# Kernel optimization log

Measured on AMD Instinct MI355X. Metric: run time of the kernel, lower is better.

## Reference

```python
import jax, jax.numpy as jnp
import numpy as np

N = 50000   # nodes
E = 800000  # edges
DIN, DH, DOUT = 128, 128, 128


def _w(k, o, i):
    return jax.random.normal(k, (o, i), jnp.float32) * (1.0 / np.sqrt(i))


def setup_inputs() -> dict:
    key = jax.random.key(0)
    ks = jax.random.split(key, 16)
    return {
        "x": jax.random.normal(ks[0], (N, DIN), jnp.float32),
        "edge_index": jax.random.randint(ks[1], (2, E), 0, N, dtype=jnp.int64),
        # conv1 = GraphSAGE(DIN, DH, num_layers=2): two SAGEConv layers
        "W1l": _w(ks[2], DH, DIN), "W1r": _w(ks[3], DH, DIN), "b1": jnp.zeros((DH,), jnp.float32),
        "W2l": _w(ks[4], DH, DH),  "W2r": _w(ks[5], DH, DH),  "b2": jnp.zeros((DH,), jnp.float32),
        # conv2 = GraphSAGE(DH, DOUT, num_layers=2)
        "W3l": _w(ks[6], DOUT, DH),   "W3r": _w(ks[7], DOUT, DH),   "b3": jnp.zeros((DOUT,), jnp.float32),
        "W4l": _w(ks[8], DOUT, DOUT), "W4r": _w(ks[9], DOUT, DOUT), "b4": jnp.zeros((DOUT,), jnp.float32),
        # final fc
        "Wfc": _w(ks[10], DOUT, DOUT), "bfc": jnp.zeros((DOUT,), jnp.float32),
    }


def _sage(x, src, dst, Wl, Wr, b):
    # PyG SAGEConv (aggr='mean'): out = lin_l(mean_{j in N(i)} x_j) + lin_r(x_i)
    agg = jax.ops.segment_sum(x[src], dst, num_segments=N)          # [N, F]
    cnt = jax.ops.segment_sum(jnp.ones((src.shape[0],), x.dtype), dst, num_segments=N)
    mean = agg / jnp.maximum(cnt, 1.0)[:, None]                     # isolated nodes -> 0
    return mean @ Wl.T + x @ Wr.T + b


def reference(x, edge_index, W1l, W1r, b1, W2l, W2r, b2,
              W3l, W3r, b3, W4l, W4r, b4, Wfc, bfc):
    src, dst = edge_index[0], edge_index[1]
    h = _sage(x, src, dst, W1l, W1r, b1)
    h = jax.nn.relu(h)                        # inter-layer act inside conv1
    h = _sage(h, src, dst, W2l, W2r, b2)
    h = jax.nn.relu(h)                        # F.relu(self.conv1(...))
    h = _sage(h, src, dst, W3l, W3r, b3)
    h = jax.nn.relu(h)                        # inter-layer act inside conv2
    h = _sage(h, src, dst, W4l, W4r, b4)
    h = jax.nn.relu(h)                        # F.relu(self.conv2(...))
    return h @ Wfc.T + bfc
```

## Files before the change

### kernel.cpp

```cpp
#include <hip/hip_runtime.h>

#define DF 128
#define SCAN_TILE 2048
#define SHP 136

typedef __attribute__((ext_vector_type(8))) short bf16x8;
typedef __attribute__((ext_vector_type(4))) float f32x4;

__device__ __forceinline__ ushort f2b(float f) {
    uint u = __float_as_uint(f);
    u += 0x7FFF + ((u >> 16) & 1);
    return (ushort)(u >> 16);
}
__device__ __forceinline__ float blo(uint v) { return __uint_as_float(v << 16); }
__device__ __forceinline__ float bhi(uint v) { return __uint_as_float(v & 0xFFFF0000u); }
__device__ __forceinline__ uint pk(float lo, float hi) {
    return (uint)f2b(lo) | ((uint)f2b(hi) << 16);
}


__global__ void zero_kernel(uint4* __restrict__ p, int n16) {
    int i = blockIdx.x * blockDim.x + threadIdx.x;
    if (i < n16) p[i] = (uint4){0u, 0u, 0u, 0u};
}


struct WPtrs { const float* p[9]; };

__global__ void prep_kernel(const int* __restrict__ dst, int* __restrict__ cnt,
                            ushort* __restrict__ rnk, int E, int CB,
                            const float* __restrict__ x, ushort* __restrict__ Xb, int n4, int XB,
                            WPtrs w, ushort* __restrict__ Wb) {
    const int b = blockIdx.x, tid = threadIdx.x;
    if (b < CB) {
        int e = b * 256 + tid;
        if (e < E) rnk[e] = (ushort)atomicAdd(&cnt[dst[e]], 1);
    } else if (b < CB + XB) {
        int i = (b - CB) * 256 + tid;
        if (i < n4) {
            float4 v = *reinterpret_cast<const float4*>(x + (long long)i * 4);
            uint2 p;
            p.x = pk(v.x, v.y);
            p.y = pk(v.z, v.w);
            *reinterpret_cast<uint2*>(Xb + (long long)i * 4) = p;
        }
    } else {
        int q = b - CB - XB;
        int m = q >> 6;
        int i = (q & 63) * 256 + tid;
        Wb[m * 16384 + i] = f2b(w.p[m][i]);
    }
}


__global__ __launch_bounds__(256) void scan_reduce(const int* __restrict__ cnt,
                                                   int* __restrict__ bsum, int N) {
    __shared__ int sw[4];
    const int tid = threadIdx.x, lane = tid & 63, wid = tid >> 6;
    const int base = blockIdx.x * SCAN_TILE + tid * 8;
    int s = 0;
    #pragma unroll
    for (int j = 0; j < 8; ++j) { int i = base + j; if (i < N) s += cnt[i]; }
    #pragma unroll
    for (int off = 1; off < 64; off <<= 1) s += __shfl_xor(s, off);
    if (lane == 0) sw[wid] = s;
    __syncthreads();
    if (tid == 0) bsum[blockIdx.x] = sw[0] + sw[1] + sw[2] + sw[3];
}

__global__ __launch_bounds__(256) void scan_apply(const int* __restrict__ cnt,
                                                  const int* __restrict__ bsum, int nb,
                                                  int* __restrict__ row_start,
                                                  float* __restrict__ inv, int N) {
    __shared__ int sw[4];
    __shared__ int sbs[64];
    __shared__ int stot;
    const int tid = threadIdx.x, lane = tid & 63, wid = tid >> 6;
    if (tid < 64) {
        int v = (lane < nb) ? bsum[lane] : 0;
        int incl = v;
        #pragma unroll
        for (int off = 1; off < 64; off <<= 1) {
            int t = __shfl_up(incl, off);
            if (lane >= off) incl += t;
        }
        sbs[lane] = incl - v;
        if (lane == 63) stot = incl;
    }
    __syncthreads();

    const int base = blockIdx.x * SCAN_TILE + tid * 8;
    int v[8];
    int tsum = 0;
    #pragma unroll
    for (int j = 0; j < 8; ++j) {
        int i = base + j;
        v[j] = (i < N) ? cnt[i] : 0;
        tsum += v[j];
    }
    int incl = tsum;
    #pragma unroll
    for (int off = 1; off < 64; off <<= 1) {
        int t = __shfl_up(incl, off);
        if (lane >= off) incl += t;
    }
    if (lane == 63) sw[wid] = incl;
    __syncthreads();
    int woff = 0;
    #pragma unroll
    for (int k = 0; k < 4; ++k) woff += (k < wid) ? sw[k] : 0;
    int run = sbs[blockIdx.x] + woff + (incl - tsum);
    #pragma unroll
    for (int j = 0; j < 8; ++j) {
        int i = base + j;
        if (i < N) {
            row_start[i] = run;
            inv[i]       = 1.0f / fmaxf((float)v[j], 1.0f);
        }
        run += v[j];
    }
    if (blockIdx.x == 0 && tid == 0) row_start[N] = stot;
}

__global__ void place_kernel(const int* __restrict__ src, const int* __restrict__ dst,
                             const int* __restrict__ row_start, const ushort* __restrict__ rnk,
                             ushort* __restrict__ col, int E) {
    int e = blockIdx.x * blockDim.x + threadIdx.x;
    if (e < E) {
        int p = row_start[dst[e]] + (int)rnk[e];
        col[p] = (ushort)src[e];
    }
}


__global__ __launch_bounds__(256) void aggregate_kernel(
        const ushort* __restrict__ H,
        const int* __restrict__ row_start, const ushort* __restrict__ col,
        const float* __restrict__ inv, ushort* __restrict__ M, int N) {
    const int node = blockIdx.x * 4 + (threadIdx.x >> 6);
    const int lane = threadIdx.x & 63;
    if (node >= N) return;
    const int s = row_start[node], e = row_start[node + 1];
    const int half = lane >> 5, l32 = lane & 31;
    const uint2* __restrict__ Hu = reinterpret_cast<const uint2*>(H);
    float a0 = 0.f, a1 = 0.f, a2 = 0.f, a3 = 0.f;
    int j = s;
    for (; j + 8 <= e; j += 8) {
        int n0 = (int)col[j + 0 + half];
        int n1 = (int)col[j + 2 + half];
        int n2 = (int)col[j + 4 + half];
        int n3 = (int)col[j + 6 + half];
        uint2 v0 = Hu[n0 * 32 + l32];
        uint2 v1 = Hu[n1 * 32 + l32];
        uint2 v2 = Hu[n2 * 32 + l32];
        uint2 v3 = Hu[n3 * 32 + l32];
        a0 += blo(v0.x); a1 += bhi(v0.x); a2 += blo(v0.y); a3 += bhi(v0.y);
        a0 += blo(v1.x); a1 += bhi(v1.x); a2 += blo(v1.y); a3 += bhi(v1.y);
        a0 += blo(v2.x); a1 += bhi(v2.x); a2 += blo(v2.y); a3 += bhi(v2.y);
        a0 += blo(v3.x); a1 += bhi(v3.x); a2 += blo(v3.y); a3 += bhi(v3.y);
    }
    for (; j + 2 <= e; j += 2) {
        int n0 = (int)col[j + half];
        uint2 v0 = Hu[n0 * 32 + l32];
        a0 += blo(v0.x); a1 += bhi(v0.x); a2 += blo(v0.y); a3 += bhi(v0.y);
    }
    if (j < e && half == 0) {
        int n0 = (int)col[j];
        uint2 v0 = Hu[n0 * 32 + l32];
        a0 += blo(v0.x); a1 += bhi(v0.x); a2 += blo(v0.y); a3 += bhi(v0.y);
    }
    a0 += __shfl_xor(a0, 32);
    a1 += __shfl_xor(a1, 32);
    a2 += __shfl_xor(a2, 32);
    a3 += __shfl_xor(a3, 32);
    if (half == 0) {
        const float iv = inv[node];
        uint2 p;
        p.x = pk(a0 * iv, a1 * iv);
        p.y = pk(a2 * iv, a3 * iv);
        reinterpret_cast<uint2*>(M + (long long)node * DF)[l32] = p;
    }
}

__device__ __forceinline__ void stage2(const ushort* __restrict__ g1,
                                       const ushort* __restrict__ g2,
                                       ushort* s1, ushort* s2, int tid) {
    bf16x8 v1[4], v2[4];
    #pragma unroll
    for (int q = 0; q < 4; ++q) {
        int idx = q * 256 + tid;
        int row = idx >> 4, ch = (idx & 15) * 8;
        v1[q] = *reinterpret_cast<const bf16x8*>(g1 + row * DF + ch);
        v2[q] = *reinterpret_cast<const bf16x8*>(g2 + row * DF + ch);
    }
    #pragma unroll
    for (int q = 0; q < 4; ++q) {
        int idx = q * 256 + tid;
        int row = idx >> 4, ch = (idx & 15) * 8;
        *reinterpret_cast<bf16x8*>(s1 + row * SHP + ch) = v1[q];
        *reinterpret_cast<bf16x8*>(s2 + row * SHP + ch) = v2[q];
    }
}


__global__ __launch_bounds__(256) void gemm_mfma(
    const ushort* __restrict__ A1,
    const ushort* __restrict__ A2,
    const ushort* __restrict__ W1,
    const ushort* __restrict__ W2,
    const float* __restrict__ bias,
    ushort* __restrict__ outB,
    int n)
{
    __shared__ ushort sA1[64 * SHP];
    __shared__ ushort sA2[64 * SHP];

    const int tid  = threadIdx.x;
    const int lane = tid & 63;
    const int w    = tid >> 6;
    const int n0   = blockIdx.x * 64;
    const int r16  = lane & 15;
    const int kq   = (lane >> 4) * 8;

    stage2(A1 + (long long)n0 * DF, A2 + (long long)n0 * DF, sA1, sA2, tid);
    __syncthreads();

    f32x4 acc[4][2];
    #pragma unroll
    for (int i = 0; i < 4; ++i)
        #pragma unroll
        for (int j = 0; j < 2; ++j) acc[i][j] = (f32x4){0.f, 0.f, 0.f, 0.f};

    #pragma unroll
    for (int pass = 0; pass < 2; ++pass) {
        const ushort* sA = pass ? sA2 : sA1;
        const ushort* W  = pass ? W2 : W1;
        #pragma unroll
        for (int kk = 0; kk < 4; ++kk) {
            const int k0 = kk * 32 + kq;
            bf16x8 b[2];
            #pragma unroll
            for (int ct = 0; ct < 2; ++ct) {
                int o = w * 32 + ct * 16 + r16;
                b[ct] = *reinterpret_cast<const bf16x8*>(W + o * DF + k0);
            }
            #pragma unroll
            for (int rt = 0; rt < 4; ++rt) {
                bf16x8 a = *reinterpret_cast<const bf16x8*>(sA + (rt * 16 + r16) * SHP + k0);
                #pragma unroll
                for (int ct = 0; ct < 2; ++ct)
                    acc[rt][ct] = __builtin_amdgcn_mfma_f32_16x16x32_bf16(a, b[ct], acc[rt][ct], 0, 0, 0);
            }
        }
    }

    #pragma unroll
    for (int rt = 0; rt < 4; ++rt) {
        #pragma unroll
        for (int ct = 0; ct < 2; ++ct) {
            const int c = w * 32 + ct * 16 + r16;
            const float bv = bias[c];
            #pragma unroll
            for (int r = 0; r < 4; ++r) {
                int row = n0 + rt * 16 + (lane >> 4) * 4 + r;
                if (row < n) {
                    float v = fmaxf(acc[rt][ct][r] + bv, 0.0f);
                    outB[(long long)row * DF + c] = f2b(v);
                }
            }
        }
    }
}


__global__ __launch_bounds__(256) void gemm_mfma_fc(
    const ushort* __restrict__ A1,
    const ushort* __restrict__ A2,
    const ushort* __restrict__ W1,
    const ushort* __restrict__ W2,
    const float* __restrict__ bias1,
    const ushort* __restrict__ Wf,
    const float* __restrict__ biasf,
    float* __restrict__ out,
    int n)
{
    __shared__ ushort sA1[64 * SHP];
    __shared__ ushort sA2[64 * SHP];

    const int tid  = threadIdx.x;
    const int lane = tid & 63;
    const int w    = tid >> 6;
    const int n0   = blockIdx.x * 64;
    const int r16  = lane & 15;
    const int kq   = (lane >> 4) * 8;

    stage2(A1 + (long long)n0 * DF, A2 + (long long)n0 * DF, sA1, sA2, tid);
    __syncthreads();

    f32x4 acc[4][2];
    #pragma unroll
    for (int i = 0; i < 4; ++i)
        #pragma unroll
        for (int j = 0; j < 2; ++j) acc[i][j] = (f32x4){0.f, 0.f, 0.f, 0.f};

    #pragma unroll
    for (int pass = 0; pass < 2; ++pass) {
        const ushort* sA = pass ? sA2 : sA1;
        const ushort* W  = pass ? W2 : W1;
        #pragma unroll
        for (int kk = 0; kk < 4; ++kk) {
            const int k0 = kk * 32 + kq;
            bf16x8 b[2];
            #pragma unroll
            for (int ct = 0; ct < 2; ++ct) {
                int o = w * 32 + ct * 16 + r16;
                b[ct] = *reinterpret_cast<const bf16x8*>(W + o * DF + k0);
            }
            #pragma unroll
            for (int rt = 0; rt < 4; ++rt) {
                bf16x8 a = *reinterpret_cast<const bf16x8*>(sA + (rt * 16 + r16) * SHP + k0);
                #pragma unroll
                for (int ct = 0; ct < 2; ++ct)
                    acc[rt][ct] = __builtin_amdgcn_mfma_f32_16x16x32_bf16(a, b[ct], acc[rt][ct], 0, 0, 0);
            }
        }
    }

    __syncthreads();

    #pragma unroll
    for (int rt = 0; rt < 4; ++rt) {
        #pragma unroll
        for (int ct = 0; ct < 2; ++ct) {
            const int c = w * 32 + ct * 16 + r16;
            const float bv = bias1[c];
            #pragma unroll
            for (int r = 0; r < 4; ++r) {
                int lrow = rt * 16 + (lane >> 4) * 4 + r;
                sA1[lrow * SHP + c] = f2b(fmaxf(acc[rt][ct][r] + bv, 0.0f));
            }
        }
    }
    __syncthreads();

    f32x4 acc2[4][2];
    #pragma unroll
    for (int i = 0; i < 4; ++i)
        #pragma unroll
        for (int j = 0; j < 2; ++j) acc2[i][j] = (f32x4){0.f, 0.f, 0.f, 0.f};

    #pragma unroll
    for (int kk = 0; kk < 4; ++kk) {
        const int k0 = kk * 32 + kq;
        bf16x8 b[2];
        #pragma unroll
        for (int ct = 0; ct < 2; ++ct) {
            int o = w * 32 + ct * 16 + r16;
            b[ct] = *reinterpret_cast<const bf16x8*>(Wf + o * DF + k0);
        }
        #pragma unroll
        for (int rt = 0; rt < 4; ++rt) {
            bf16x8 a = *reinterpret_cast<const bf16x8*>(&sA1[(rt * 16 + r16) * SHP + k0]);
            #pragma unroll
            for (int ct = 0; ct < 2; ++ct)
                acc2[rt][ct] = __builtin_amdgcn_mfma_f32_16x16x32_bf16(a, b[ct], acc2[rt][ct], 0, 0, 0);
        }
    }

    #pragma unroll
    for (int rt = 0; rt < 4; ++rt) {
        #pragma unroll
        for (int ct = 0; ct < 2; ++ct) {
            const int c = w * 32 + ct * 16 + r16;
            const float bv = biasf[c];
            #pragma unroll
            for (int r = 0; r < 4; ++r) {
                int row = n0 + rt * 16 + (lane >> 4) * 4 + r;
                if (row < n)
                    out[(long long)row * DF + c] = acc2[rt][ct][r] + bv;
            }
        }
    }
}

extern "C" void kernel_launch(void* const* d_in, const int* in_sizes, int n_in,
                              void* d_out, int out_size, void* d_ws, size_t ws_size,
                              hipStream_t stream) {
    const float* x  = (const float*)d_in[0];
    const int*   ei = (const int*)d_in[1];
    const int N = in_sizes[0] / DF;
    const int E = in_sizes[1] / 2;
    const int* src = ei;
    const int* dst = ei + E;

    const float* b1  = (const float*)d_in[4];
    const float* b2  = (const float*)d_in[7];
    const float* b3  = (const float*)d_in[10];
    const float* b4  = (const float*)d_in[13];
    const float* bfc = (const float*)d_in[15];

    float* out = (float*)d_out;

    char* ws = (char*)d_ws;
    size_t off = 0;
    auto alloc = [&](size_t bytes) { char* p = ws + off; off = (off + bytes + 255) & ~(size_t)255; return p; };
    int*    cnt       = (int*)   alloc((size_t)N * 4);
    int*    row_start = (int*)   alloc((size_t)(N + 1) * 4);
    float*  inv       = (float*) alloc((size_t)N * 4);
    int*    bsum      = (int*)   alloc(256 * 4);
    ushort* rnk       = (ushort*)alloc((size_t)E * 2);
    ushort* col       = (ushort*)alloc((size_t)E * 2);
    ushort* Xb        = (ushort*)alloc((size_t)N * DF * 2);
    ushort* M         = (ushort*)alloc((size_t)N * DF * 2);
    ushort* H         = (ushort*)alloc((size_t)N * DF * 2);
    ushort* Wb        = (ushort*)alloc((size_t)9 * 16384 * 2);
    (void)alloc(65536);

    const int n16 = (N + 3) / 4;
    zero_kernel<<<dim3((n16 + 255) / 256), dim3(256), 0, stream>>>((uint4*)cnt, n16);

    const int n4 = N * DF / 4;
    const int CB = (E + 255) / 256;
    const int XB = (n4 + 255) / 256;
    const int WB = 9 * 64;
    WPtrs wp;
    wp.p[0] = (const float*)d_in[2];  wp.p[1] = (const float*)d_in[3];
    wp.p[2] = (const float*)d_in[5];  wp.p[3] = (const float*)d_in[6];
    wp.p[4] = (const float*)d_in[8];  wp.p[5] = (const float*)d_in[9];
    wp.p[6] = (const float*)d_in[11]; wp.p[7] = (const float*)d_in[12];
    wp.p[8] = (const float*)d_in[14];
    prep_kernel<<<dim3(CB + XB + WB), dim3(256), 0, stream>>>(dst, cnt, rnk, E, CB, x, Xb, n4, XB, wp, Wb);

    const int nb = (N + SCAN_TILE - 1) / SCAN_TILE;
    scan_reduce<<<dim3(nb), dim3(256), 0, stream>>>(cnt, bsum, N);
    scan_apply<<<dim3(nb), dim3(256), 0, stream>>>(cnt, bsum, nb, row_start, inv, N);
    place_kernel<<<dim3(CB), dim3(256), 0, stream>>>(src, dst, row_start, rnk, col, E);

    const int agrid = (N + 3) / 4;
    const int ggrid = (N + 63) / 64;

    aggregate_kernel<<<dim3(agrid), dim3(256), 0, stream>>>(Xb, row_start, col, inv, M, N);
    gemm_mfma<<<dim3(ggrid), dim3(256), 0, stream>>>(M, Xb, Wb + 0*16384, Wb + 1*16384, b1, H, N);
    aggregate_kernel<<<dim3(agrid), dim3(256), 0, stream>>>(H, row_start, col, inv, M, N);
    gemm_mfma<<<dim3(ggrid), dim3(256), 0, stream>>>(M, H, Wb + 2*16384, Wb + 3*16384, b2, H, N);
    aggregate_kernel<<<dim3(agrid), dim3(256), 0, stream>>>(H, row_start, col, inv, M, N);
    gemm_mfma<<<dim3(ggrid), dim3(256), 0, stream>>>(M, H, Wb + 4*16384, Wb + 5*16384, b3, H, N);
    aggregate_kernel<<<dim3(agrid), dim3(256), 0, stream>>>(H, row_start, col, inv, M, N);
    gemm_mfma_fc<<<dim3(ggrid), dim3(256), 0, stream>>>(M, H, Wb + 6*16384, Wb + 7*16384, b4,
                                                        Wb + 8*16384, bfc, out, N);
}
```

Before: 271.3 us.

## Split degree-count atomics across eight partitioned counter arrays

The per-destination degree counting atomics are spread over eight copies of the counter array, chosen by block index, to reduce contention on hot counters. The scan kernels sum the partitions and compute per-partition offsets, and the placement kernel adds the partition offset to the rank, with the partition id packed into the upper bits of the 16-bit rank. This adds eight times the counter memory to zero, read and write, and assumes each partition's count per node stays below 256.

```diff
diff --git a/kernel.cpp b/kernel.cpp
--- a/kernel.cpp
+++ b/kernel.cpp
@@ -27,14 +27,18 @@
 
 struct WPtrs { const float* p[9]; };
 
-__global__ void prep_kernel(const int* __restrict__ dst, int* __restrict__ cnt,
+__global__ void prep_kernel(const int* __restrict__ dst, int* __restrict__ cntp, int Nr,
                             ushort* __restrict__ rnk, int E, int CB,
                             const float* __restrict__ x, ushort* __restrict__ Xb, int n4, int XB,
                             WPtrs w, ushort* __restrict__ Wb) {
     const int b = blockIdx.x, tid = threadIdx.x;
     if (b < CB) {
         int e = b * 256 + tid;
-        if (e < E) rnk[e] = (ushort)atomicAdd(&cnt[dst[e]], 1);
+        if (e < E) {
+            int part = b & 7;
+            int r = atomicAdd(&cntp[part * Nr + dst[e]], 1);
+            rnk[e] = (ushort)(r | (part << 8));
+        }
     } else if (b < CB + XB) {
         int i = (b - CB) * 256 + tid;
         if (i < n4) {
@@ -53,14 +57,24 @@
 }
 
 
-__global__ __launch_bounds__(256) void scan_reduce(const int* __restrict__ cnt,
+__global__ __launch_bounds__(256) void scan_reduce(const int* __restrict__ cntp, int Nr,
+                                                   int* __restrict__ cnt,
                                                    int* __restrict__ bsum, int N) {
     __shared__ int sw[4];
     const int tid = threadIdx.x, lane = tid & 63, wid = tid >> 6;
     const int base = blockIdx.x * SCAN_TILE + tid * 8;
     int s = 0;
     #pragma unroll
-    for (int j = 0; j < 8; ++j) { int i = base + j; if (i < N) s += cnt[i]; }
+    for (int j = 0; j < 8; ++j) {
+        int i = base + j;
+        if (i < N) {
+            int t = 0;
+            #pragma unroll
+            for (int xp = 0; xp < 8; ++xp) t += cntp[xp * Nr + i];
+            cnt[i] = t;
+            s += t;
+        }
+    }
     #pragma unroll
     for (int off = 1; off < 64; off <<= 1) s += __shfl_xor(s, off);
     if (lane == 0) sw[wid] = s;
@@ -69,6 +83,8 @@
 }
 
 __global__ __launch_bounds__(256) void scan_apply(const int* __restrict__ cnt,
+                                                  const int* __restrict__ cntp, int Nr,
+                                                  int* __restrict__ offp,
                                                   const int* __restrict__ bsum, int nb,
                                                   int* __restrict__ row_start,
                                                   float* __restrict__ inv, int N) {
@@ -116,6 +132,12 @@
         if (i < N) {
             row_start[i] = run;
             inv[i]       = 1.0f / fmaxf((float)v[j], 1.0f);
+            int acc = 0;
+            #pragma unroll
+            for (int xp = 0; xp < 8; ++xp) {
+                offp[xp * Nr + i] = acc;
+                acc += cntp[xp * Nr + i];
+            }
         }
         run += v[j];
     }
@@ -123,11 +145,15 @@
 }
 
 __global__ void place_kernel(const int* __restrict__ src, const int* __restrict__ dst,
-                             const int* __restrict__ row_start, const ushort* __restrict__ rnk,
+                             const int* __restrict__ row_start,
+                             const int* __restrict__ offp, int Nr,
+                             const ushort* __restrict__ rnk,
                              ushort* __restrict__ col, int E) {
     int e = blockIdx.x * blockDim.x + threadIdx.x;
     if (e < E) {
-        int p = row_start[dst[e]] + (int)rnk[e];
+        int d  = dst[e];
+        int rv = (int)rnk[e];
+        int p  = row_start[d] + offp[(rv >> 8) * Nr + d] + (rv & 255);
         col[p] = (ushort)src[e];
     }
 }
@@ -401,9 +427,12 @@
 
     float* out = (float*)d_out;
 
+    const int Nr = (N + 255) & ~255;
     char* ws = (char*)d_ws;
     size_t off = 0;
     auto alloc = [&](size_t bytes) { char* p = ws + off; off = (off + bytes + 255) & ~(size_t)255; return p; };
+    int*    cntp      = (int*)   alloc((size_t)8 * Nr * 4);
+    int*    offp      = (int*)   alloc((size_t)8 * Nr * 4);
     int*    cnt       = (int*)   alloc((size_t)N * 4);
     int*    row_start = (int*)   alloc((size_t)(N + 1) * 4);
     float*  inv       = (float*) alloc((size_t)N * 4);
@@ -416,8 +445,8 @@
     ushort* Wb        = (ushort*)alloc((size_t)9 * 16384 * 2);
     (void)alloc(65536);
 
-    const int n16 = (N + 3) / 4;
-    zero_kernel<<<dim3((n16 + 255) / 256), dim3(256), 0, stream>>>((uint4*)cnt, n16);
+    const int n16 = 8 * Nr / 4;
+    zero_kernel<<<dim3((n16 + 255) / 256), dim3(256), 0, stream>>>((uint4*)cntp, n16);
 
     const int n4 = N * DF / 4;
     const int CB = (E + 255) / 256;
@@ -429,12 +458,13 @@
     wp.p[4] = (const float*)d_in[8];  wp.p[5] = (const float*)d_in[9];
     wp.p[6] = (const float*)d_in[11]; wp.p[7] = (const float*)d_in[12];
     wp.p[8] = (const float*)d_in[14];
-    prep_kernel<<<dim3(CB + XB + WB), dim3(256), 0, stream>>>(dst, cnt, rnk, E, CB, x, Xb, n4, XB, wp, Wb);
+    prep_kernel<<<dim3(CB + XB + WB), dim3(256), 0, stream>>>(dst, cntp, Nr, rnk, E, CB,
+                                                              x, Xb, n4, XB, wp, Wb);
 
     const int nb = (N + SCAN_TILE - 1) / SCAN_TILE;
-    scan_reduce<<<dim3(nb), dim3(256), 0, stream>>>(cnt, bsum, N);
-    scan_apply<<<dim3(nb), dim3(256), 0, stream>>>(cnt, bsum, nb, row_start, inv, N);
-    place_kernel<<<dim3(CB), dim3(256), 0, stream>>>(src, dst, row_start, rnk, col, E);
+    scan_reduce<<<dim3(nb), dim3(256), 0, stream>>>(cntp, Nr, cnt, bsum, N);
+    scan_apply<<<dim3(nb), dim3(256), 0, stream>>>(cnt, cntp, Nr, offp, bsum, nb, row_start, inv, N);
+    place_kernel<<<dim3(CB), dim3(256), 0, stream>>>(src, dst, row_start, offp, Nr, rnk, col, E);
 
     const int agrid = (N + 3) / 4;
     const int ggrid = (N + 63) / 64;
```

Result: slower. 288.4 us (+6.3%).
